# Kernel optimization log

Hardware: AMD Instinct MI355X
Metric: run time of the kernel (lower is better)

The kernel has to match this reference:

```python
import jax, jax.numpy as jnp
import numpy as np

HEADS = 16


def bemm(x, weight, bias, er, es):
    # BatchEnsembleMM.forward: x [T,B,Hin], weight [Hout,Hin], er [B,Hin], es [B,Hout]
    x_r = x * er[None, :, :]
    x_mm = jnp.einsum('tbh,oh->tbo', x_r, weight)
    return x_mm * es[None, :, :] + bias


def rel_shift(x):
    # RelativeShift.forward (batch_first): x [N, len_q, len_r]
    n, q, r = x.shape
    x_pad = jnp.pad(x, ((0, 0), (0, 0), (1, 0)))        # [N, q, r+1]
    x_view = x_pad.reshape(n, r + 1, q)[:, 1:, :]        # drop first 'row'
    return x_view.reshape(n, q, r)


def setup_inputs() -> dict:
    key = jax.random.key(0)
    ks = jax.random.split(key, 14)
    T, B, H = 1024, 8, 1024
    Lr = 1024
    s = 0.02
    return {
        'inputs': jax.random.normal(ks[0], (T, B, H), jnp.float32),
        'pos': jax.random.normal(ks[1], (Lr, 1, H), jnp.float32),
        'input_weights': jax.random.normal(ks[2], (3 * H, H), jnp.float32) * s,
        'input_biases': jax.random.normal(ks[3], (3 * H,), jnp.float32) * s,
        'pos_weights': jax.random.normal(ks[4], (H, H), jnp.float32) * s,
        'pos_biases': jax.random.normal(ks[5], (H,), jnp.float32) * s,
        'output_weights': jax.random.normal(ks[6], (H, H), jnp.float32) * s,
        'output_biases': jax.random.normal(ks[7], (H,), jnp.float32) * s,
        'r_i': 1.0 + jax.random.normal(ks[8], (B, H), jnp.float32) * 0.1,
        's_i': 1.0 + jax.random.normal(ks[9], (B, 3 * H), jnp.float32) * 0.1,
        'r_p': 1.0 + jax.random.normal(ks[10], (B, H), jnp.float32) * 0.1,
        's_p': 1.0 + jax.random.normal(ks[11], (B, H), jnp.float32) * 0.1,
        'r_w_bias': jax.random.normal(ks[12], (HEADS, H // HEADS), jnp.float32) * s,
        'r_r_bias': jax.random.normal(ks[13], (HEADS, H // HEADS), jnp.float32) * s,
        'heads': HEADS,
    }


def reference(inputs, pos, input_weights, input_biases, pos_weights, pos_biases,
              output_weights, output_biases, r_i, s_i, r_p, s_p,
              r_w_bias, r_r_bias, heads):
    T, B, H = inputs.shape
    hd = H // heads
    scale = hd ** (-0.5)
    Lr = pos.shape[0]

    pos_rep = jnp.broadcast_to(pos, (Lr, B, H))

    # BatchEnsemble QKV and positional projections (training path)
    qkv = bemm(inputs, input_weights, input_biases, r_i, s_i)       # [T,B,3H]
    qkv = qkv.reshape(T, B * heads, 3, hd)
    queries, keys, values = qkv[:, :, 0, :], qkv[:, :, 1, :], qkv[:, :, 2, :]

    r_head_k = bemm(pos_rep, pos_weights, pos_biases, r_p, s_p)     # [Lr,B,H]
    r_head_k = r_head_k.reshape(Lr, B * heads, hd)

    rw_head_q = (queries.reshape(T, B, heads, hd) + r_w_bias).reshape(T, B * heads, hd)
    rr_head_q = (queries.reshape(T, B, heads, hd) + r_r_bias).reshape(T, B * heads, hd)

    # content score AC and position score BD
    matmul_ac = jnp.einsum('qnd,knd->nqk', rw_head_q, keys) * scale    # [B*h,T,T]
    matmul_bd = jnp.einsum('qnd,rnd->nqr', rr_head_q, r_head_k) * scale
    matmul_bd = rel_shift(matmul_bd)[:, :, :T]

    attn_score = matmul_ac + matmul_bd
    softmax_results = jax.nn.softmax(attn_score.astype(jnp.float32), axis=-1).astype(inputs.dtype)

    context = jnp.einsum('nqk,knd->qnd', softmax_results, values).reshape(T, B, H)
    outputs = jnp.einsum('tbh,oh->tbo', context, output_weights) + output_biases
    return outputs
```

## Files before the change

kernel.cpp:

```cpp
#include <hip/hip_runtime.h>
#include <cstdint>
#include <cstddef>

using u16 = unsigned short;
typedef short short8 __attribute__((ext_vector_type(8)));
typedef short short4v __attribute__((ext_vector_type(4)));
typedef unsigned short us8 __attribute__((ext_vector_type(8)));
typedef unsigned short us4 __attribute__((ext_vector_type(4)));
typedef float f32x4 __attribute__((ext_vector_type(4)));
typedef float f4 __attribute__((ext_vector_type(4)));

#define T_ 1024
#define B_ 8
#define H_ 1024
#define HEADS_ 16
#define HD_ 64
#define N3_ 3072

__device__ __forceinline__ float b2f(u16 u){
  union { float f; unsigned int i; } v; v.i = ((unsigned int)u) << 16; return v.f;
}
__device__ __forceinline__ u16 f2b(float f){
  union { float f; unsigned int i; } v; v.f = f;
  return (u16)((v.i + 0x8000u) >> 16);
}
typedef __attribute__((address_space(1))) const void gvoid;
typedef __attribute__((address_space(3))) void lvoid;
__device__ __forceinline__ void gload16(const void* g, void* l){
  __builtin_amdgcn_global_load_lds((gvoid*)g, (lvoid*)l, 16, 0, 0);
}

__global__ __launch_bounds__(256) void k_scaleA(const float* __restrict__ x, const float* __restrict__ r,
                                                u16* __restrict__ o){
  int idx = blockIdx.x * 256 + threadIdx.x;
  int base = idx * 8;
  int h = base & (H_ - 1);
  int b = (base >> 10) & (B_ - 1);
  f4 x0 = *(const f4*)(x + base), x1 = *(const f4*)(x + base + 4);
  f4 r0 = *(const f4*)(r + b * H_ + h), r1 = *(const f4*)(r + b * H_ + h + 4);
  us8 ov;
#pragma unroll
  for (int u = 0; u < 4; ++u){ ov[u] = f2b(x0[u] * r0[u]); ov[u + 4] = f2b(x1[u] * r1[u]); }
  *(us8*)(o + base) = ov;
}

template<bool HAS_S, bool SCALE_A, bool POS_A, bool A_BF16, bool OUT_F32>
__global__ __launch_bounds__(256) void k_gemm(const void* __restrict__ A_, const float* __restrict__ W,
                                              const float* __restrict__ RA, const float* __restrict__ S,
                                              const float* __restrict__ bias, void* __restrict__ C_, int N){
  const int K = 1024;
  const int n0 = blockIdx.x * 128, m0 = blockIdx.y * 128;
  const int tid = threadIdx.x, lane = tid & 63;
  const int wave = tid >> 6, wr = wave >> 1, wc = wave & 1;
  __shared__ alignas(16) u16 At[128 * 32];
  __shared__ alignas(16) u16 Bt[128 * 32];
  f32x4 acc[4][4] = {};

  for (int kt = 0; kt < 32; ++kt){
    const int k0 = kt * 32;
    f4 wv[4];
    f4 avf[4];
#pragma unroll
    for (int i = 0; i < 4; ++i){
      int c = tid + i * 256, r = c >> 3, sg = c & 7;
      wv[i] = *(const f4*)(W + (size_t)(n0 + r) * K + k0 + sg * 4);
    }
    if (!A_BF16){
      const float* A = (const float*)A_;
#pragma unroll
      for (int i = 0; i < 4; ++i){
        int c = tid + i * 256, r = c >> 3, sg = c & 7;
        int m = m0 + r;
        const float* ap = POS_A ? (A + (size_t)(m >> 3) * K + k0 + sg * 4)
                                : (A + (size_t)m * K + k0 + sg * 4);
        avf[i] = *(const f4*)ap;
        if (SCALE_A){
          f4 rv = *(const f4*)(RA + (m & 7) * K + k0 + sg * 4);
          avf[i] = avf[i] * rv;
        }
      }
    }
    __syncthreads();
    if (A_BF16){
      const u16* A = (const u16*)A_;
#pragma unroll
      for (int i = 0; i < 2; ++i){
        int c = tid + i * 256, r = c >> 2, sg = c & 3;
        gload16(A + (size_t)(m0 + r) * K + k0 + sg * 8, (char*)At + (size_t)c * 16);
      }
    }
#pragma unroll
    for (int i = 0; i < 4; ++i){
      int c = tid + i * 256, r = c >> 3, sg = c & 7;
      us4 pw;
#pragma unroll
      for (int u = 0; u < 4; ++u) pw[u] = f2b(wv[i][u]);
      *(us4*)(Bt + r * 32 + sg * 4) = pw;
    }
    if (!A_BF16){
#pragma unroll
      for (int i = 0; i < 4; ++i){
        int c = tid + i * 256, r = c >> 3, sg = c & 7;
        us4 pa;
#pragma unroll
        for (int u = 0; u < 4; ++u) pa[u] = f2b(avf[i][u]);
        *(us4*)(At + r * 32 + sg * 4) = pa;
      }
    }
    __syncthreads();
    short8 af[4], bf[4];
#pragma unroll
    for (int i = 0; i < 4; ++i){
      int ar = wr * 64 + i * 16 + (lane & 15);
      af[i] = *(const short8*)(At + ar * 32 + ((lane >> 4) << 3));
      int br = wc * 64 + i * 16 + (lane & 15);
      bf[i] = *(const short8*)(Bt + br * 32 + ((lane >> 4) << 3));
    }
#pragma unroll
    for (int i = 0; i < 4; ++i)
#pragma unroll
      for (int j = 0; j < 4; ++j)
        acc[i][j] = __builtin_amdgcn_mfma_f32_16x16x32_bf16(af[i], bf[j], acc[i][j], 0, 0, 0);
  }
#pragma unroll
  for (int i = 0; i < 4; ++i){
    int row0 = wr * 64 + i * 16 + ((lane >> 4) << 2);
#pragma unroll
    for (int j = 0; j < 4; ++j){
      int o = n0 + wc * 64 + j * 16 + (lane & 15);
      float bv = bias[o];
#pragma unroll
      for (int jj = 0; jj < 4; ++jj){
        int m = m0 + row0 + jj;
        float v = acc[i][j][jj];
        if (HAS_S) v *= S[(m & 7) * N + o];
        v += bv;
        if (OUT_F32) ((float*)C_)[(size_t)m * N + o] = v;
        else         ((u16*)C_)[(size_t)m * N + o] = f2b(v);
      }
    }
  }
}

__global__ __launch_bounds__(256) void k_vt(const u16* __restrict__ qkv, u16* __restrict__ VT){
  const int tt = blockIdx.x;
  const int n = blockIdx.y;
  const int b = n >> 4, head = n & 15;
  __shared__ alignas(16) u16 tile[64][72];
  const int tid = threadIdx.x;
#pragma unroll
  for (int i = 0; i < 2; ++i){
    int c = tid + i * 256;
    int r = c >> 3, sg = c & 7;
    const u16* src = qkv + ((size_t)(tt * 64 + r) * 8 + b) * N3_ + head * 192 + 128 + sg * 8;
    *(us8*)&tile[r][sg * 8] = *(const us8*)src;
  }
  __syncthreads();
#pragma unroll
  for (int i = 0; i < 2; ++i){
    int c = tid + i * 256;
    int d = c >> 3, sg = c & 7;
    us8 ov;
#pragma unroll
    for (int u = 0; u < 8; ++u) ov[u] = tile[sg * 8 + u][d];
    *(us8*)(VT + ((size_t)n * 64 + d) * 1024 + tt * 64 + sg * 8) = ov;
  }
}

#define G_OFF   0
#define RWQ_OFF 67664
#define RRQ_OFF 71760
#define RED_OFF 77904
#define SMEM_SZ 79952

__global__ __launch_bounds__(512) __attribute__((amdgpu_waves_per_eu(4, 4)))
void k_attn(const u16* __restrict__ qkv, const u16* __restrict__ rk,
            const u16* __restrict__ VTg, const float* __restrict__ rwb,
            const float* __restrict__ rrb, u16* __restrict__ ctx){
  const int bid = blockIdx.x;
  const int n = (bid & 7) + ((bid >> 8) << 3);
  const int qb = (bid >> 3) & 31;
  const int q0 = qb * 32;
  const int bat = n >> 4, head = n & 15;
  const int tid = threadIdx.x, lane = tid & 63, wave = tid >> 6;
  const int l15 = lane & 15, grp = lane >> 4;

  __shared__ alignas(16) char smem[SMEM_SZ];
  char* gB  = smem + G_OFF;
  u16* rwq = (u16*)(smem + RWQ_OFF);
  u16* rrq = (u16*)(smem + RRQ_OFF);
  float* redf = (float*)(smem + RED_OFF);

  const float PRESCALE = 0.125f * 1.44269504089f;
#pragma unroll
  for (int rep = 0; rep < 2; ++rep){
    int c = tid + rep * 512;
    if (c < 640){
      int s = c >> 3, sg = c & 7;
      u16* dst; int row; const float* bias;
      if (s < 32){ dst = rwq; row = s; bias = rwb; }
      else       { dst = rrq; row = s - 32; bias = rrb; }
      int qrow = q0 + row;
      float v[8];
      const float* bp2 = bias + head * 64 + sg * 8;
      if (qrow < T_){
        const u16* qp = qkv + ((size_t)qrow * 8 + bat) * N3_ + head * 192 + sg * 8;
        us8 qv = *(const us8*)qp;
        f4 b0 = *(const f4*)bp2, b1 = *(const f4*)(bp2 + 4);
#pragma unroll
        for (int u = 0; u < 4; ++u){
          v[u]     = (b2f(qv[u])     + b0[u]) * PRESCALE;
          v[u + 4] = (b2f(qv[u + 4]) + b1[u]) * PRESCALE;
        }
      } else {
#pragma unroll
        for (int u = 0; u < 8; ++u) v[u] = 0.f;
      }
      us8 pk;
#pragma unroll
      for (int u = 0; u < 8; ++u) pk[u] = f2b(v[u]);
      *(us8*)((char*)dst + row * 128 + ((sg * 16) ^ ((row & 7) << 4))) = pk;
    }
  }
  if (tid < 33) *(u16*)(gB + tid * 2050 + 2048) = 0;

  auto ldf = [&](const void* base, int row, int kkb)->short8 {
    int co = kkb + (grp << 4);
    return *(const short8*)((const char*)base + row * 128 + (co ^ ((row & 7) << 4)));
  };

  __syncthreads();

  {
    short8 af[3][2];
#pragma unroll
    for (int pi = 0; pi < 3; ++pi)
#pragma unroll
      for (int kk = 0; kk < 2; ++kk) af[pi][kk] = ldf(rrq, pi * 16 + l15, kk * 64);
    const int sbase = (grp * 4) * 2050 + ((wave * 64 + l15) << 1);
#pragma unroll
    for (int s = 0; s < 2; ++s){
#pragma unroll
      for (int c4 = 0; c4 < 4; ++c4){
        int r = s * 512 + wave * 64 + c4 * 16 + l15;
        const u16* bp = rk + ((size_t)r * 8 + bat) * 1024 + head * 64 + grp * 8;
        short8 bf0 = *(const short8*)bp;
        short8 bf1 = *(const short8*)(bp + 32);
        __builtin_amdgcn_s_setprio(1);
#pragma unroll
        for (int pi = 0; pi < 3; ++pi){
          f32x4 acc = {0.f, 0.f, 0.f, 0.f};
          acc = __builtin_amdgcn_mfma_f32_16x16x32_bf16(af[pi][0], bf0, acc, 0, 0, 0);
          acc = __builtin_amdgcn_mfma_f32_16x16x32_bf16(af[pi][1], bf1, acc, 0, 0, 0);
#pragma unroll
          for (int jj = 0; jj < 4; ++jj){
            int a = pi * 16 + (grp << 2) + jj;
            if (a < 33)
              *(u16*)(gB + sbase + (pi * 16 + jj) * 2050 + ((s * 512 + c4 * 16) << 1)) = f2b(acc[jj]);
          }
        }
        __builtin_amdgcn_s_setprio(0);
      }
    }
  }
  __syncthreads();

  short8 qf[2][2];
#pragma unroll
  for (int m = 0; m < 2; ++m)
#pragma unroll
    for (int kk = 0; kk < 2; ++kk) qf[m][kk] = ldf(rwq, m * 16 + l15, kk * 64);

  float m_run[2] = {-3.0e38f, -3.0e38f};
  float l_run[2] = {0.f, 0.f};
  f32x4 Oacc[2][4] = {};

  const int gthr = (l15 << 11) + ((1023 - q0 + wave * 64 + (grp << 2)) << 1);

#pragma unroll
  for (int pr = 0; pr < 4; ++pr){
    int base = wave * 64 + (pr & 1) * 32 + (pr >> 1) * 512;
    short8 kf[2][2];
#pragma unroll
    for (int h = 0; h < 2; ++h){
      const u16* kp = qkv + ((size_t)(base + h * 16 + l15) * 8 + bat) * N3_ + head * 192 + 64 + grp * 8;
      kf[h][0] = *(const short8*)kp;
      kf[h][1] = *(const short8*)(kp + 32);
    }
    short8 vb[4];
#pragma unroll
    for (int dt = 0; dt < 4; ++dt){
      const u16* vp = VTg + ((size_t)n * 64 + dt * 16 + l15) * 1024 + base + (grp << 2);
      *(short4v*)&vb[dt] = *(const short4v*)vp;
      *((short4v*)&vb[dt] + 1) = *(const short4v*)(vp + 16);
    }
    float s_[2][2][4];
#pragma unroll
    for (int h = 0; h < 2; ++h){
      __builtin_amdgcn_s_setprio(1);
      f32x4 acc0 = {0.f, 0.f, 0.f, 0.f}, acc1 = {0.f, 0.f, 0.f, 0.f};
      acc0 = __builtin_amdgcn_mfma_f32_16x16x32_bf16(kf[h][0], qf[0][0], acc0, 0, 0, 0);
      acc0 = __builtin_amdgcn_mfma_f32_16x16x32_bf16(kf[h][1], qf[0][1], acc0, 0, 0, 0);
      acc1 = __builtin_amdgcn_mfma_f32_16x16x32_bf16(kf[h][0], qf[1][0], acc1, 0, 0, 0);
      acc1 = __builtin_amdgcn_mfma_f32_16x16x32_bf16(kf[h][1], qf[1][1], acc1, 0, 0, 0);
      __builtin_amdgcn_s_setprio(0);
#pragma unroll
      for (int jj = 0; jj < 4; ++jj){
        int coff = (((pr & 1) * 32 + (pr >> 1) * 512 + h * 16 + jj) << 1);
        s_[h][0][jj] = acc0[jj] + b2f(*(const u16*)(gB + gthr + coff));
        s_[h][1][jj] = acc1[jj] + b2f(*(const u16*)(gB + gthr + (1 << 15) + coff));
      }
    }
    float cm[2];
#pragma unroll
    for (int m = 0; m < 2; ++m){
      float c0 = fmaxf(fmaxf(s_[0][m][0], s_[0][m][1]), fmaxf(s_[0][m][2], s_[0][m][3]));
      float c1 = fmaxf(fmaxf(s_[1][m][0], s_[1][m][1]), fmaxf(s_[1][m][2], s_[1][m][3]));
      float c = fmaxf(c0, c1);
      c = fmaxf(c, __shfl_xor(c, 16));
      c = fmaxf(c, __shfl_xor(c, 32));
      cm[m] = c;
    }
    if (!__all(cm[0] <= m_run[0] + 8.f && cm[1] <= m_run[1] + 8.f)){
#pragma unroll
      for (int m = 0; m < 2; ++m){
        float mn = fmaxf(m_run[m], cm[m]);
        float f = __builtin_exp2f(m_run[m] - mn);
        l_run[m] *= f;
        m_run[m] = mn;
#pragma unroll
        for (int jj = 0; jj < 4; ++jj){
          float fq = __shfl(f, (lane & 48) + ((lane >> 2) & 12) + jj);
#pragma unroll
          for (int dt = 0; dt < 4; ++dt) Oacc[m][dt][jj] *= fq;
        }
      }
    }
    short8 pa[2];
#pragma unroll
    for (int m = 0; m < 2; ++m){
      float ls = 0.f;
#pragma unroll
      for (int jj = 0; jj < 4; ++jj){
        float e0 = __builtin_exp2f(s_[0][m][jj] - m_run[m]);
        float e1 = __builtin_exp2f(s_[1][m][jj] - m_run[m]);
        ls += e0 + e1;
        pa[m][jj]     = (short)f2b(e0);
        pa[m][4 + jj] = (short)f2b(e1);
      }
      l_run[m] += ls;
    }
    __builtin_amdgcn_s_setprio(1);
#pragma unroll
    for (int dt = 0; dt < 4; ++dt)
#pragma unroll
      for (int m = 0; m < 2; ++m)
        Oacc[m][dt] = __builtin_amdgcn_mfma_f32_16x16x32_bf16(pa[m], vb[dt], Oacc[m][dt], 0, 0, 0);
    __builtin_amdgcn_s_setprio(0);
  }

#pragma unroll
  for (int m = 0; m < 2; ++m){
    l_run[m] += __shfl_xor(l_run[m], 16);
    l_run[m] += __shfl_xor(l_run[m], 32);
  }
  if (grp == 0){
#pragma unroll
    for (int m = 0; m < 2; ++m){
      redf[wave * 32 + m * 16 + l15] = m_run[m];
      redf[256 + wave * 32 + m * 16 + l15] = l_run[m];
    }
  }
  __syncthreads();

  float* par = (float*)(smem + wave * 8192);
#pragma unroll
  for (int m = 0; m < 2; ++m)
#pragma unroll
    for (int dt = 0; dt < 4; ++dt)
#pragma unroll
      for (int jj = 0; jj < 4; ++jj)
        par[(m * 16 + (grp << 2) + jj) * 64 + dt * 16 + l15] = Oacc[m][dt][jj];
  __syncthreads();

  {
    float* parAll = (float*)smem;
    int q = tid >> 4, d4 = (tid & 15) * 4;
    float M = -3.0e38f;
#pragma unroll
    for (int w = 0; w < 8; ++w) M = fmaxf(M, redf[w * 32 + q]);
    f32x4 v = {0.f, 0.f, 0.f, 0.f};
    float L = 0.f;
#pragma unroll
    for (int w = 0; w < 8; ++w){
      float sc = __builtin_exp2f(redf[w * 32 + q] - M);
      L += redf[256 + w * 32 + q] * sc;
      f32x4 pv = *(const f32x4*)(parAll + w * 2048 + q * 64 + d4);
      v += pv * sc;
    }
    float il = 1.0f / (L + 1e-20f);
    us4 pk;
#pragma unroll
    for (int e = 0; e < 4; ++e) pk[e] = f2b(v[e] * il);
    *(us4*)(ctx + ((size_t)(q0 + q) * 8 + bat) * 1024 + head * 64 + d4) = pk;
  }
}

extern "C" void kernel_launch(void* const* d_in, const int* in_sizes, int n_in,
                              void* d_out, int out_size, void* d_ws, size_t ws_size,
                              hipStream_t stream){
  const float* x   = (const float*)d_in[0];
  const float* pos = (const float*)d_in[1];
  const float* Wi  = (const float*)d_in[2];
  const float* bi  = (const float*)d_in[3];
  const float* Wp  = (const float*)d_in[4];
  const float* bp  = (const float*)d_in[5];
  const float* Wo  = (const float*)d_in[6];
  const float* bo  = (const float*)d_in[7];
  const float* r_i = (const float*)d_in[8];
  const float* s_i = (const float*)d_in[9];
  const float* r_p = (const float*)d_in[10];
  const float* s_p = (const float*)d_in[11];
  const float* rwb = (const float*)d_in[12];
  const float* rrb = (const float*)d_in[13];

  const size_t MB = 1024 * 1024;
  u16* qkv = (u16*)((char*)d_ws);
  u16* rk  = (u16*)((char*)d_ws + 48 * MB);
  u16* Ai   = (u16*)d_out;
  u16* VTg  = (u16*)d_out;
  u16* ctxg = (u16*)((char*)d_out + 16777216);

  k_scaleA<<<dim3(4096), 256, 0, stream>>>(x, r_i, Ai);
  k_gemm<true,  false, false, true,  false><<<dim3(24, 64), 256, 0, stream>>>(Ai,  Wi, nullptr, s_i, bi, qkv, N3_);
  k_gemm<true,  true,  true,  false, false><<<dim3(8, 64),  256, 0, stream>>>(pos, Wp, r_p,    s_p, bp, rk, 1024);
  k_vt<<<dim3(16, 128), 256, 0, stream>>>(qkv, VTg);
  k_attn<<<dim3(4096), 512, 0, stream>>>(qkv, rk, VTg, rwb, rrb, ctxg);
  hipMemcpyAsync(qkv, ctxg, (size_t)out_size * sizeof(u16), hipMemcpyDeviceToDevice, stream);
  k_gemm<false, false, false, true,  true ><<<dim3(8, 64),  256, 0, stream>>>(qkv, Wo, nullptr, nullptr, bo, (float*)d_out, 1024);
}
```

Before: 439.8 us.

## Halve attention query tile to 16 rows for higher occupancy

The attention kernel now handles 16 query rows per block instead of 32, doubling the grid to 8192 blocks. LDS use drops from about 80KB to 42KB and register pressure falls, and the waves-per-EU hint is raised from 4 to 6-8 so more blocks fit per CU. The rel-shift BD tile shrinks to 17 rows with a one-column offset, and the gB reads are vectorised into a single us4 load. The cost is that every K/V tile and positional-key tile is reloaded and recomputed twice as often, so global traffic and redundant BD MFMA work per query row rise.

```diff
diff --git a/kernel.cpp b/kernel.cpp
--- a/kernel.cpp
+++ b/kernel.cpp
@@ -168,19 +168,19 @@
 }
 
 #define G_OFF   0
-#define RWQ_OFF 67664
-#define RRQ_OFF 71760
-#define RED_OFF 77904
-#define SMEM_SZ 79952
-
-__global__ __launch_bounds__(512) __attribute__((amdgpu_waves_per_eu(4, 4)))
+#define RWQ_OFF 34864
+#define RRQ_OFF 36912
+#define RED_OFF 41008
+#define SMEM_SZ 42032
+
+__global__ __launch_bounds__(512) __attribute__((amdgpu_waves_per_eu(6, 8)))
 void k_attn(const u16* __restrict__ qkv, const u16* __restrict__ rk,
             const u16* __restrict__ VTg, const float* __restrict__ rwb,
             const float* __restrict__ rrb, u16* __restrict__ ctx){
   const int bid = blockIdx.x;
-  const int n = (bid & 7) + ((bid >> 8) << 3);
-  const int qb = (bid >> 3) & 31;
-  const int q0 = qb * 32;
+  const int n = (bid & 7) + ((bid >> 9) << 3);
+  const int qb = (bid >> 3) & 63;
+  const int q0 = qb * 16;
   const int bat = n >> 4, head = n & 15;
   const int tid = threadIdx.x, lane = tid & 63, wave = tid >> 6;
   const int l15 = lane & 15, grp = lane >> 4;
@@ -192,37 +192,34 @@
   float* redf = (float*)(smem + RED_OFF);
 
   const float PRESCALE = 0.125f * 1.44269504089f;
-#pragma unroll
-  for (int rep = 0; rep < 2; ++rep){
-    int c = tid + rep * 512;
-    if (c < 640){
-      int s = c >> 3, sg = c & 7;
-      u16* dst; int row; const float* bias;
-      if (s < 32){ dst = rwq; row = s; bias = rwb; }
-      else       { dst = rrq; row = s - 32; bias = rrb; }
-      int qrow = q0 + row;
-      float v[8];
-      const float* bp2 = bias + head * 64 + sg * 8;
-      if (qrow < T_){
-        const u16* qp = qkv + ((size_t)qrow * 8 + bat) * N3_ + head * 192 + sg * 8;
-        us8 qv = *(const us8*)qp;
-        f4 b0 = *(const f4*)bp2, b1 = *(const f4*)(bp2 + 4);
-#pragma unroll
-        for (int u = 0; u < 4; ++u){
-          v[u]     = (b2f(qv[u])     + b0[u]) * PRESCALE;
-          v[u + 4] = (b2f(qv[u + 4]) + b1[u]) * PRESCALE;
-        }
-      } else {
-#pragma unroll
-        for (int u = 0; u < 8; ++u) v[u] = 0.f;
-      }
-      us8 pk;
-#pragma unroll
-      for (int u = 0; u < 8; ++u) pk[u] = f2b(v[u]);
-      *(us8*)((char*)dst + row * 128 + ((sg * 16) ^ ((row & 7) << 4))) = pk;
-    }
-  }
-  if (tid < 33) *(u16*)(gB + tid * 2050 + 2048) = 0;
+  if (tid < 384){
+    int s = tid >> 3, sg = tid & 7;
+    u16* dst; int row; const float* bias;
+    if (s < 16){ dst = rwq; row = s; bias = rwb; }
+    else       { dst = rrq; row = s - 16; bias = rrb; }
+    int qrow = q0 + row;
+    float v[8];
+    const float* bp2 = bias + head * 64 + sg * 8;
+    bool live = (qrow < T_) && (dst == rwq || row < 17);
+    if (live){
+      const u16* qp = qkv + ((size_t)qrow * 8 + bat) * N3_ + head * 192 + sg * 8;
+      us8 qv = *(const us8*)qp;
+      f4 b0 = *(const f4*)bp2, b1 = *(const f4*)(bp2 + 4);
+#pragma unroll
+      for (int u = 0; u < 4; ++u){
+        v[u]     = (b2f(qv[u])     + b0[u]) * PRESCALE;
+        v[u + 4] = (b2f(qv[u + 4]) + b1[u]) * PRESCALE;
+      }
+    } else {
+#pragma unroll
+      for (int u = 0; u < 8; ++u) v[u] = 0.f;
+    }
+    us8 pk;
+#pragma unroll
+    for (int u = 0; u < 8; ++u) pk[u] = f2b(v[u]);
+    *(us8*)((char*)dst + row * 128 + ((sg * 16) ^ ((row & 7) << 4))) = pk;
+  }
+  if (tid < 17) *(u16*)(gB + tid * 2050) = 0;
 
   auto ldf = [&](const void* base, int row, int kkb)->short8 {
     int co = kkb + (grp << 4);
@@ -232,12 +229,12 @@
   __syncthreads();
 
   {
-    short8 af[3][2];
-#pragma unroll
-    for (int pi = 0; pi < 3; ++pi)
+    short8 af[2][2];
+#pragma unroll
+    for (int pi = 0; pi < 2; ++pi)
 #pragma unroll
       for (int kk = 0; kk < 2; ++kk) af[pi][kk] = ldf(rrq, pi * 16 + l15, kk * 64);
-    const int sbase = (grp * 4) * 2050 + ((wave * 64 + l15) << 1);
+    const int sbase = (grp * 4) * 2050 + ((wave * 64 + l15) << 1) + 2;
 #pragma unroll
     for (int s = 0; s < 2; ++s){
 #pragma unroll
@@ -248,14 +245,14 @@
         short8 bf1 = *(const short8*)(bp + 32);
         __builtin_amdgcn_s_setprio(1);
 #pragma unroll
-        for (int pi = 0; pi < 3; ++pi){
+        for (int pi = 0; pi < 2; ++pi){
           f32x4 acc = {0.f, 0.f, 0.f, 0.f};
           acc = __builtin_amdgcn_mfma_f32_16x16x32_bf16(af[pi][0], bf0, acc, 0, 0, 0);
           acc = __builtin_amdgcn_mfma_f32_16x16x32_bf16(af[pi][1], bf1, acc, 0, 0, 0);
 #pragma unroll
           for (int jj = 0; jj < 4; ++jj){
             int a = pi * 16 + (grp << 2) + jj;
-            if (a < 33)
+            if (a < 17)
               *(u16*)(gB + sbase + (pi * 16 + jj) * 2050 + ((s * 512 + c4 * 16) << 1)) = f2b(acc[jj]);
           }
         }
@@ -265,17 +262,15 @@
   }
   __syncthreads();
 
-  short8 qf[2][2];
-#pragma unroll
-  for (int m = 0; m < 2; ++m)
-#pragma unroll
-    for (int kk = 0; kk < 2; ++kk) qf[m][kk] = ldf(rwq, m * 16 + l15, kk * 64);
-
-  float m_run[2] = {-3.0e38f, -3.0e38f};
-  float l_run[2] = {0.f, 0.f};
-  f32x4 Oacc[2][4] = {};
-
-  const int gthr = (l15 << 11) + ((1023 - q0 + wave * 64 + (grp << 2)) << 1);
+  short8 qf[2];
+#pragma unroll
+  for (int kk = 0; kk < 2; ++kk) qf[kk] = ldf(rwq, l15, kk * 64);
+
+  float m_run = -3.0e38f;
+  float l_run = 0.f;
+  f32x4 Oacc[4] = {};
+
+  const int gthr = (l15 << 11) + ((1024 - q0 + wave * 64 + (grp << 2)) << 1);
 
 #pragma unroll
   for (int pr = 0; pr < 4; ++pr){
@@ -294,115 +289,86 @@
       *(short4v*)&vb[dt] = *(const short4v*)vp;
       *((short4v*)&vb[dt] + 1) = *(const short4v*)(vp + 16);
     }
-    float s_[2][2][4];
+    float s_[2][4];
 #pragma unroll
     for (int h = 0; h < 2; ++h){
       __builtin_amdgcn_s_setprio(1);
-      f32x4 acc0 = {0.f, 0.f, 0.f, 0.f}, acc1 = {0.f, 0.f, 0.f, 0.f};
-      acc0 = __builtin_amdgcn_mfma_f32_16x16x32_bf16(kf[h][0], qf[0][0], acc0, 0, 0, 0);
-      acc0 = __builtin_amdgcn_mfma_f32_16x16x32_bf16(kf[h][1], qf[0][1], acc0, 0, 0, 0);
-      acc1 = __builtin_amdgcn_mfma_f32_16x16x32_bf16(kf[h][0], qf[1][0], acc1, 0, 0, 0);
-      acc1 = __builtin_amdgcn_mfma_f32_16x16x32_bf16(kf[h][1], qf[1][1], acc1, 0, 0, 0);
+      f32x4 acc = {0.f, 0.f, 0.f, 0.f};
+      acc = __builtin_amdgcn_mfma_f32_16x16x32_bf16(kf[h][0], qf[0], acc, 0, 0, 0);
+      acc = __builtin_amdgcn_mfma_f32_16x16x32_bf16(kf[h][1], qf[1], acc, 0, 0, 0);
       __builtin_amdgcn_s_setprio(0);
+      us4 g4 = *(const us4*)(gB + gthr + (((pr & 1) * 32 + (pr >> 1) * 512 + h * 16) << 1));
+#pragma unroll
+      for (int jj = 0; jj < 4; ++jj) s_[h][jj] = acc[jj] + b2f(g4[jj]);
+    }
+    float c0 = fmaxf(fmaxf(s_[0][0], s_[0][1]), fmaxf(s_[0][2], s_[0][3]));
+    float c1 = fmaxf(fmaxf(s_[1][0], s_[1][1]), fmaxf(s_[1][2], s_[1][3]));
+    float cm = fmaxf(c0, c1);
+    cm = fmaxf(cm, __shfl_xor(cm, 16));
+    cm = fmaxf(cm, __shfl_xor(cm, 32));
+    if (!__all(cm <= m_run + 8.f)){
+      float mn = fmaxf(m_run, cm);
+      float f = __builtin_exp2f(m_run - mn);
+      l_run *= f;
+      m_run = mn;
 #pragma unroll
       for (int jj = 0; jj < 4; ++jj){
-        int coff = (((pr & 1) * 32 + (pr >> 1) * 512 + h * 16 + jj) << 1);
-        s_[h][0][jj] = acc0[jj] + b2f(*(const u16*)(gB + gthr + coff));
-        s_[h][1][jj] = acc1[jj] + b2f(*(const u16*)(gB + gthr + (1 << 15) + coff));
-      }
-    }
-    float cm[2];
-#pragma unroll
-    for (int m = 0; m < 2; ++m){
-      float c0 = fmaxf(fmaxf(s_[0][m][0], s_[0][m][1]), fmaxf(s_[0][m][2], s_[0][m][3]));
-      float c1 = fmaxf(fmaxf(s_[1][m][0], s_[1][m][1]), fmaxf(s_[1][m][2], s_[1][m][3]));
-      float c = fmaxf(c0, c1);
-      c = fmaxf(c, __shfl_xor(c, 16));
-      c = fmaxf(c, __shfl_xor(c, 32));
-      cm[m] = c;
-    }
-    if (!__all(cm[0] <= m_run[0] + 8.f && cm[1] <= m_run[1] + 8.f)){
-#pragma unroll
-      for (int m = 0; m < 2; ++m){
-        float mn = fmaxf(m_run[m], cm[m]);
-        float f = __builtin_exp2f(m_run[m] - mn);
-        l_run[m] *= f;
-        m_run[m] = mn;
-#pragma unroll
-        for (int jj = 0; jj < 4; ++jj){
-          float fq = __shfl(f, (lane & 48) + ((lane >> 2) & 12) + jj);
-#pragma unroll
-          for (int dt = 0; dt < 4; ++dt) Oacc[m][dt][jj] *= fq;
-        }
-      }
-    }
-    short8 pa[2];
-#pragma unroll
-    for (int m = 0; m < 2; ++m){
-      float ls = 0.f;
-#pragma unroll
-      for (int jj = 0; jj < 4; ++jj){
-        float e0 = __builtin_exp2f(s_[0][m][jj] - m_run[m]);
-        float e1 = __builtin_exp2f(s_[1][m][jj] - m_run[m]);
-        ls += e0 + e1;
-        pa[m][jj]     = (short)f2b(e0);
-        pa[m][4 + jj] = (short)f2b(e1);
-      }
-      l_run[m] += ls;
-    }
+        float fq = __shfl(f, (lane & 48) + ((lane >> 2) & 12) + jj);
+#pragma unroll
+        for (int dt = 0; dt < 4; ++dt) Oacc[dt][jj] *= fq;
+      }
+    }
+    short8 pa;
+    float ls = 0.f;
+#pragma unroll
+    for (int jj = 0; jj < 4; ++jj){
+      float e0 = __builtin_exp2f(s_[0][jj] - m_run);
+      float e1 = __builtin_exp2f(s_[1][jj] - m_run);
+      ls += e0 + e1;
+      pa[jj]     = (short)f2b(e0);
+      pa[4 + jj] = (short)f2b(e1);
+    }
+    l_run += ls;
     __builtin_amdgcn_s_setprio(1);
 #pragma unroll
     for (int dt = 0; dt < 4; ++dt)
-#pragma unroll
-      for (int m = 0; m < 2; ++m)
-        Oacc[m][dt] = __builtin_amdgcn_mfma_f32_16x16x32_bf16(pa[m], vb[dt], Oacc[m][dt], 0, 0, 0);
+      Oacc[dt] = __builtin_amdgcn_mfma_f32_16x16x32_bf16(pa, vb[dt], Oacc[dt], 0, 0, 0);
     __builtin_amdgcn_s_setprio(0);
   }
 
-#pragma unroll
-  for (int m = 0; m < 2; ++m){
-    l_run[m] += __shfl_xor(l_run[m], 16);
-    l_run[m] += __shfl_xor(l_run[m], 32);
-  }
+  l_run += __shfl_xor(l_run, 16);
+  l_run += __shfl_xor(l_run, 32);
   if (grp == 0){
-#pragma unroll
-    for (int m = 0; m < 2; ++m){
-      redf[wave * 32 + m * 16 + l15] = m_run[m];
-      redf[256 + wave * 32 + m * 16 + l15] = l_run[m];
-    }
+    redf[wave * 16 + l15] = m_run;
+    redf[128 + wave * 16 + l15] = l_run;
   }
   __syncthreads();
 
-  float* par = (float*)(smem + wave * 8192);
-#pragma unroll
-  for (int m = 0; m < 2; ++m)
-#pragma unroll
-    for (int dt = 0; dt < 4; ++dt)
-#pragma unroll
-      for (int jj = 0; jj < 4; ++jj)
-        par[(m * 16 + (grp << 2) + jj) * 64 + dt * 16 + l15] = Oacc[m][dt][jj];
+  float* par = (float*)(smem + wave * 4096);
+#pragma unroll
+  for (int dt = 0; dt < 4; ++dt)
+#pragma unroll
+    for (int jj = 0; jj < 4; ++jj)
+      par[((grp << 2) + jj) * 64 + dt * 16 + l15] = Oacc[dt][jj];
   __syncthreads();
 
   {
     float* parAll = (float*)smem;
-    int q = tid >> 4, d4 = (tid & 15) * 4;
+    int q = tid >> 5, dp = (tid & 31) * 2;
     float M = -3.0e38f;
 #pragma unroll
-    for (int w = 0; w < 8; ++w) M = fmaxf(M, redf[w * 32 + q]);
-    f32x4 v = {0.f, 0.f, 0.f, 0.f};
-    float L = 0.f;
+    for (int w = 0; w < 8; ++w) M = fmaxf(M, redf[w * 16 + q]);
+    float v0 = 0.f, v1 = 0.f, L = 0.f;
 #pragma unroll
     for (int w = 0; w < 8; ++w){
-      float sc = __builtin_exp2f(redf[w * 32 + q] - M);
-      L += redf[256 + w * 32 + q] * sc;
-      f32x4 pv = *(const f32x4*)(parAll + w * 2048 + q * 64 + d4);
-      v += pv * sc;
+      float sc = __builtin_exp2f(redf[w * 16 + q] - M);
+      L += redf[128 + w * 16 + q] * sc;
+      const float* pw = parAll + w * 1024 + q * 64 + dp;
+      v0 += pw[0] * sc; v1 += pw[1] * sc;
     }
     float il = 1.0f / (L + 1e-20f);
-    us4 pk;
-#pragma unroll
-    for (int e = 0; e < 4; ++e) pk[e] = f2b(v[e] * il);
-    *(us4*)(ctx + ((size_t)(q0 + q) * 8 + bat) * 1024 + head * 64 + d4) = pk;
+    unsigned int pk = (unsigned int)f2b(v0 * il) | ((unsigned int)f2b(v1 * il) << 16);
+    *(unsigned int*)(ctx + ((size_t)(q0 + q) * 8 + bat) * 1024 + head * 64 + dp) = pk;
   }
 }
 
@@ -435,7 +401,7 @@
   k_gemm<true,  false, false, true,  false><<<dim3(24, 64), 256, 0, stream>>>(Ai,  Wi, nullptr, s_i, bi, qkv, N3_);
   k_gemm<true,  true,  true,  false, false><<<dim3(8, 64),  256, 0, stream>>>(pos, Wp, r_p,    s_p, bp, rk, 1024);
   k_vt<<<dim3(16, 128), 256, 0, stream>>>(qkv, VTg);
-  k_attn<<<dim3(4096), 512, 0, stream>>>(qkv, rk, VTg, rwb, rrb, ctxg);
+  k_attn<<<dim3(8192), 512, 0, stream>>>(qkv, rk, VTg, rwb, rrb, ctxg);
   hipMemcpyAsync(qkv, ctxg, (size_t)out_size * sizeof(u16), hipMemcpyDeviceToDevice, stream);
   k_gemm<false, false, false, true,  true ><<<dim3(8, 64),  256, 0, stream>>>(qkv, Wo, nullptr, nullptr, bo, (float*)d_out, 1024);
 }
```

After: 679.2 us. +54.4%, slower.
